# Performance work log

Hardware: AMD Instinct MI355X
Metric: run time of the kernel (lower is better)

The kernel has to match this reference:

```python
import jax, jax.numpy as jnp
import numpy as np

HEADS = 16


def setup_inputs() -> dict:
    key = jax.random.key(0)
    k1, k2, k3 = jax.random.split(key, 3)
    B, T, D = 2, 2048, 1024
    x = jax.random.normal(k1, (B, T, D), dtype=jnp.float32)
    # causal mask, broadcast over batch and heads
    mask = jnp.tril(jnp.ones((T, T), dtype=bool))[None, None, :, :]
    # torch Linear(dim, 3*dim, bias=False): weight [3D, D]; we store transposed [D, 3D]
    Wqkv = jax.random.normal(k2, (D, 3 * D), dtype=jnp.float32) * (D ** -0.5)
    Wo = jax.random.normal(k3, (D, D), dtype=jnp.float32) * (D ** -0.5)
    return {"x": x, "mask": mask, "Wqkv": Wqkv, "Wo": Wo}


def reference(x, mask, Wqkv, Wo):
    B, T, D = x.shape
    h = HEADS
    dh = D // h
    scale = dh ** -0.5
    qkv = (x @ Wqkv).reshape(B, T, 3, h, dh)
    qkv = jnp.transpose(qkv, (2, 0, 3, 1, 4))  # [3, B, h, T, dh]
    q, k, v = qkv[0], qkv[1], qkv[2]
    att = jnp.einsum("bhqd,bhkd->bhqk", q, k) * scale  # [B, h, T, T]
    att = jnp.where(mask, att, jnp.float32(-1e9))
    att = jax.nn.softmax(att, axis=-1)
    # dropout: identity in eval/reference mode
    out = jnp.einsum("bhqk,bhkd->bhqd", att, v)  # [B, h, T, dh]
    out = jnp.transpose(out, (0, 2, 1, 3)).reshape(B, T, D)
    return out @ Wo
```

## Files before the change

kernel.cpp:

```cpp
#include <hip/hip_runtime.h>
#include <cstdint>

typedef unsigned short ushort_t;
typedef __attribute__((ext_vector_type(8))) short short8;
typedef __attribute__((ext_vector_type(4))) float f32x4;

#define B_ 2
#define T_ 2048
#define D_ 1024
#define H_ 16
#define DH_ 64

__device__ inline unsigned short f2bf(float f) {
  unsigned int u = __float_as_uint(f);
  u += 0x7FFF + ((u >> 16) & 1);
  return (unsigned short)(u >> 16);
}

__device__ inline unsigned short f2bf_fast(float f) {
  return (unsigned short)((__float_as_uint(f) + 0x8000u) >> 16);
}

__device__ inline f32x4 mfma16(short8 a, short8 b, f32x4 c) {
  return __builtin_amdgcn_mfma_f32_16x16x32_bf16(a, b, c, 0, 0, 0);
}

__device__ inline void gload16(const void* g, void* l) {
  __builtin_amdgcn_global_load_lds(
      (const __attribute__((address_space(1))) unsigned int*)(uintptr_t)g,
      (__attribute__((address_space(3))) unsigned int*)(uint32_t)(uintptr_t)l,
      16, 0, 0);
}

__global__ void k_cvt(const float* __restrict__ in, ushort_t* __restrict__ out, int n4) {
  int i = blockIdx.x * blockDim.x + threadIdx.x;
  if (i >= n4) return;
  float4 v = ((const float4*)in)[i];
  ushort4 o;
  o.x = f2bf(v.x); o.y = f2bf(v.y); o.z = f2bf(v.z); o.w = f2bf(v.w);
  ((ushort4*)out)[i] = o;
}

__global__ void k_tcvt(const float* __restrict__ in, ushort_t* __restrict__ out,
                       int R, int C) {
  __shared__ float tile[32][33];
  int c0 = blockIdx.x * 32, r0 = blockIdx.y * 32;
  int tx = threadIdx.x, ty = threadIdx.y;
#pragma unroll
  for (int i = 0; i < 32; i += 8)
    tile[ty + i][tx] = in[(size_t)(r0 + ty + i) * C + c0 + tx];
  __syncthreads();
#pragma unroll
  for (int i = 0; i < 32; i += 8)
    out[(size_t)(c0 + ty + i) * R + r0 + tx] = f2bf(tile[tx][ty + i]);
}

__global__ void k_pack_qk(const ushort_t* __restrict__ qkv,
                          ushort_t* __restrict__ pq, ushort_t* __restrict__ pk) {
  const int t16 = blockIdx.x, bh = blockIdx.y;
  const int b = bh >> 4, hh = bh & 15;
  const int tsel = threadIdx.x >> 6;
  const int l = threadIdx.x & 63;
  const int lrow = l & 15, lg = l >> 4;
  ushort_t* dst = (tsel ? pk : pq) + (size_t)(bh * 128 + t16) * 1024 + l * 8;
  const ushort_t* src = qkv + (size_t)(b * T_ + t16 * 16 + lrow) * (3 * D_)
                        + tsel * D_ + hh * DH_ + lg * 8;
  short8 v0 = *(const short8*)(src);
  short8 v1 = *(const short8*)(src + 32);
  if (tsel == 0) {
    const float SC = 0.125f * 1.44269504f;
#pragma unroll
    for (int i = 0; i < 8; ++i) {
      float f0 = __uint_as_float(((unsigned)(unsigned short)v0[i]) << 16) * SC;
      float f1 = __uint_as_float(((unsigned)(unsigned short)v1[i]) << 16) * SC;
      v0[i] = (short)f2bf(f0);
      v1[i] = (short)f2bf(f1);
    }
  }
  *(short8*)(dst)       = v0;
  *(short8*)(dst + 512) = v1;
}

__global__ void k_pack_v(const ushort_t* __restrict__ qkv, ushort_t* __restrict__ pv) {
  __shared__ ushort_t tile[32][68];
  const int t32 = blockIdx.x, bh = blockIdx.y;
  const int b = bh >> 4, hh = bh & 15;
  const int t = threadIdx.x;
  {
    const int row = t >> 3, ch = t & 7;
    *(short8*)&tile[row][ch * 8] =
        *(const short8*)(qkv + (size_t)(b * T_ + t32 * 32 + row) * (3 * D_)
                         + 2 * D_ + hh * DH_ + ch * 8);
  }
  __syncthreads();
  const int nt = t >> 6, l = t & 63;
  const int lrow = l & 15, lg = l >> 4;
  const int d = nt * 16 + lrow;
  short8 o;
#pragma unroll
  for (int i = 0; i < 8; ++i) o[i] = (short)tile[lg * 8 + i][d];
  *(short8*)(pv + ((size_t)(bh * 64 + t32) * 4 + nt) * 512 + l * 8) = o;
}

template <int OUTF>
__global__ __launch_bounds__(256, 2) void k_gemm_bt(
    const ushort_t* __restrict__ A, const ushort_t* __restrict__ Bt,
    void* __restrict__ C, int M, int N, int K) {
  __shared__ __align__(16) ushort_t As[128 * 32];
  __shared__ __align__(16) ushort_t Bs[128 * 32];
  const int tid = threadIdx.x;
  const int w = tid >> 6, l = tid & 63;
  const int bm = blockIdx.y, bn = blockIdx.x;
  const int wm = w >> 1, wn = w & 1;

  const f32x4 fz = {0.f, 0.f, 0.f, 0.f};
  f32x4 acc[4][4];
#pragma unroll
  for (int i = 0; i < 4; ++i)
#pragma unroll
    for (int j = 0; j < 4; ++j) acc[i][j] = fz;

  const int r_a = l >> 2;
  const int cb = (l & 3) * 16;
  const int lrow = l & 15;
  const int lk16 = (l >> 4) * 16;

  for (int k0 = 0; k0 < K; k0 += 32) {
    __syncthreads();
#pragma unroll
    for (int c = 0; c < 2; ++c) {
      int row = (w * 2 + c) * 16 + r_a;
      gload16((const char*)A + ((size_t)(bm * 128 + row) * K + k0) * 2 + cb,
              (char*)As + row * 64 + cb);
      gload16((const char*)Bt + ((size_t)(bn * 128 + row) * K + k0) * 2 + cb,
              (char*)Bs + row * 64 + cb);
    }
    __syncthreads();
    short8 af[4], bv[4];
#pragma unroll
    for (int mt = 0; mt < 4; ++mt)
      af[mt] = *(const short8*)((const char*)As + (wm * 64 + mt * 16 + lrow) * 64 + lk16);
#pragma unroll
    for (int nt = 0; nt < 4; ++nt)
      bv[nt] = *(const short8*)((const char*)Bs + (wn * 64 + nt * 16 + lrow) * 64 + lk16);
#pragma unroll
    for (int mt = 0; mt < 4; ++mt)
#pragma unroll
      for (int nt = 0; nt < 4; ++nt)
        acc[mt][nt] = mfma16(af[mt], bv[nt], acc[mt][nt]);
  }

  const int rg = (l >> 4) * 4;
#pragma unroll
  for (int mt = 0; mt < 4; ++mt)
#pragma unroll
    for (int nt = 0; nt < 4; ++nt) {
      size_t col = (size_t)bn * 128 + wn * 64 + nt * 16 + lrow;
#pragma unroll
      for (int r = 0; r < 4; ++r) {
        size_t rowi = (size_t)bm * 128 + wm * 64 + mt * 16 + rg + r;
        if (OUTF)
          ((float*)C)[rowi * N + col] = acc[mt][nt][r];
        else
          ((ushort_t*)C)[rowi * N + col] = f2bf(acc[mt][nt][r]);
      }
    }
}

__global__ __launch_bounds__(128) void k_attn(
    const ushort_t* __restrict__ pq, const ushort_t* __restrict__ pk,
    const ushort_t* __restrict__ pv, ushort_t* __restrict__ ctx) {
  __shared__ __align__(16) ushort_t plds[2][16][72];
  const int tid = threadIdx.x;
  const int w = tid >> 6, l = tid & 63;
  const int n = blockIdx.x;
  const int q = n >> 3;
  const int bh = (n & 7) * 4 + (q & 3);
  const int j = (63 - (q >> 2)) * 2 + w;
  const int b = bh >> 4, hh = bh & 15;
  const int qr0 = j * 16;
  const int lrow = l & 15, lg = l >> 4;

  const ushort_t* pqb = pq + (size_t)(bh * 128 + j) * 1024 + l * 8;
  short8 aq0 = *(const short8*)(pqb);
  short8 aq1 = *(const short8*)(pqb + 512);

  const f32x4 fz = {0.f, 0.f, 0.f, 0.f};
  f32x4 o[4];
#pragma unroll
  for (int nt = 0; nt < 4; ++nt) o[nt] = fz;
  float lsum[4] = {0.f, 0.f, 0.f, 0.f};

  const int ntiles = (j >> 2) + 1;
  for (int t = 0; t < ntiles; ++t) {
    const int kv0 = t * 64;
    const ushort_t* pkb = pk + (size_t)(bh * 128 + (kv0 >> 4)) * 1024 + l * 8;
    short8 bk0[4], bk1[4];
#pragma unroll
    for (int nh = 0; nh < 4; ++nh) {
      bk0[nh] = *(const short8*)(pkb + nh * 1024);
      bk1[nh] = *(const short8*)(pkb + nh * 1024 + 512);
    }
    f32x4 s[4];
    __builtin_amdgcn_s_setprio(1);
#pragma unroll
    for (int nh = 0; nh < 4; ++nh)
      s[nh] = mfma16(aq1, bk1[nh], mfma16(aq0, bk0[nh], fz));
    __builtin_amdgcn_s_setprio(0);
    if (t == ntiles - 1) {
#pragma unroll
      for (int r = 0; r < 4; ++r) {
        int row = qr0 + lg * 4 + r;
#pragma unroll
        for (int nh = 0; nh < 4; ++nh) {
          int col = kv0 + nh * 16 + lrow;
          if (col > row) s[nh][r] = -1e30f;
        }
      }
    }
    const ushort_t* pvb = pv + (size_t)(bh * 64 + (kv0 >> 5)) * 2048 + l * 8;
    short8 bv0[4], bv1[4];
#pragma unroll
    for (int nt = 0; nt < 4; ++nt) {
      bv0[nt] = *(const short8*)(pvb + nt * 512);
      bv1[nt] = *(const short8*)(pvb + 2048 + nt * 512);
    }
#pragma unroll
    for (int r = 0; r < 4; ++r) {
      float p0 = __builtin_amdgcn_exp2f(s[0][r]);
      float p1 = __builtin_amdgcn_exp2f(s[1][r]);
      float p2 = __builtin_amdgcn_exp2f(s[2][r]);
      float p3 = __builtin_amdgcn_exp2f(s[3][r]);
      lsum[r] += (p0 + p1) + (p2 + p3);
      plds[w][lg * 4 + r][lrow]      = f2bf_fast(p0);
      plds[w][lg * 4 + r][16 + lrow] = f2bf_fast(p1);
      plds[w][lg * 4 + r][32 + lrow] = f2bf_fast(p2);
      plds[w][lg * 4 + r][48 + lrow] = f2bf_fast(p3);
    }
    short8 pa0 = *(const short8*)&plds[w][lrow][lg * 8];
    short8 pa1 = *(const short8*)&plds[w][lrow][32 + lg * 8];
    __builtin_amdgcn_s_setprio(1);
#pragma unroll
    for (int nt = 0; nt < 4; ++nt)
      o[nt] = mfma16(pa1, bv1[nt], mfma16(pa0, bv0[nt], o[nt]));
    __builtin_amdgcn_s_setprio(0);
  }
#pragma unroll
  for (int r = 0; r < 4; ++r)
#pragma unroll
    for (int x = 1; x < 16; x <<= 1)
      lsum[r] += __shfl_xor(lsum[r], x);
#pragma unroll
  for (int nt = 0; nt < 4; ++nt) {
#pragma unroll
    for (int r = 0; r < 4; ++r) {
      int row = qr0 + lg * 4 + r;
      ctx[(size_t)(b * T_ + row) * D_ + hh * DH_ + nt * 16 + lrow] =
          f2bf(o[nt][r] / lsum[r]);
    }
  }
}

extern "C" void kernel_launch(void* const* d_in, const int* in_sizes, int n_in,
                              void* d_out, int out_size, void* d_ws, size_t ws_size,
                              hipStream_t stream) {
  const float* x    = (const float*)d_in[0];
  const float* Wqkv = (const float*)d_in[2];
  const float* Wo   = (const float*)d_in[3];
  float* out = (float*)d_out;

  char* ws = (char*)d_ws;
  ushort_t* xb    = (ushort_t*)(ws);
  ushort_t* wqkvT = (ushort_t*)(ws + (8u  << 20));
  ushort_t* woT   = (ushort_t*)(ws + (14u << 20));
  ushort_t* qkvb  = (ushort_t*)(ws + (16u << 20));
  ushort_t* pq    = (ushort_t*)(ws + (40u << 20));
  ushort_t* pk    = (ushort_t*)(ws + (48u << 20));
  ushort_t* pv    = (ushort_t*)(ws);
  ushort_t* ctxb  = (ushort_t*)(ws + (16u << 20));

  dim3 tb(32, 8);
  k_cvt<<<(B_ * T_ * D_) / 4 / 256, 256, 0, stream>>>(x, xb, (B_ * T_ * D_) / 4);
  k_tcvt<<<dim3(96, 32), tb, 0, stream>>>(Wqkv, wqkvT, 1024, 3072);
  k_tcvt<<<dim3(32, 32), tb, 0, stream>>>(Wo, woT, 1024, 1024);
  k_gemm_bt<0><<<dim3(24, 32), 256, 0, stream>>>(xb, wqkvT, qkvb, 4096, 3072, 1024);
  k_pack_qk<<<dim3(128, 32), 128, 0, stream>>>(qkvb, pq, pk);
  k_pack_v<<<dim3(64, 32), 256, 0, stream>>>(qkvb, pv);
  k_attn<<<2048, 128, 0, stream>>>(pq, pk, pv, ctxb);
  k_gemm_bt<1><<<dim3(8, 32), 256, 0, stream>>>(ctxb, woT, out, 4096, 1024, 1024);
}
```

Before: 204.6 us.

## Process two 16-row query tiles per wave in attention to reuse K/V loads

Each wave now handles 32 query rows (two 16-row tiles) instead of 16. Every loaded K and V fragment then feeds twice as many MFMAs, and the grid is halved to 1024 blocks. This cuts global K/V traffic per query row but raises register pressure and halves the number of waves. Causal imbalance also gets coarser, since each wave loops over tiles up to its higher row group and does extra masked work for the first tile.

```diff
diff --git a/kernel.cpp b/kernel.cpp
--- a/kernel.cpp
+++ b/kernel.cpp
@@ -170,28 +170,32 @@
 __global__ __launch_bounds__(128) void k_attn(
     const ushort_t* __restrict__ pq, const ushort_t* __restrict__ pk,
     const ushort_t* __restrict__ pv, ushort_t* __restrict__ ctx) {
-  __shared__ __align__(16) ushort_t plds[2][16][72];
+  __shared__ __align__(16) ushort_t plds[2][2][16][72];
   const int tid = threadIdx.x;
   const int w = tid >> 6, l = tid & 63;
   const int n = blockIdx.x;
   const int q = n >> 3;
   const int bh = (n & 7) * 4 + (q & 3);
-  const int j = (63 - (q >> 2)) * 2 + w;
+  const int j2 = (31 - (q >> 2)) * 2 + w;
   const int b = bh >> 4, hh = bh & 15;
-  const int qr0 = j * 16;
+  const int jlo = j2 * 2;
+  const int qr0 = jlo * 16;
   const int lrow = l & 15, lg = l >> 4;
 
-  const ushort_t* pqb = pq + (size_t)(bh * 128 + j) * 1024 + l * 8;
-  short8 aq0 = *(const short8*)(pqb);
-  short8 aq1 = *(const short8*)(pqb + 512);
+  const ushort_t* pqb = pq + (size_t)(bh * 128 + jlo) * 1024 + l * 8;
+  short8 aq00 = *(const short8*)(pqb);
+  short8 aq01 = *(const short8*)(pqb + 512);
+  short8 aq10 = *(const short8*)(pqb + 1024);
+  short8 aq11 = *(const short8*)(pqb + 1536);
 
   const f32x4 fz = {0.f, 0.f, 0.f, 0.f};
-  f32x4 o[4];
-#pragma unroll
-  for (int nt = 0; nt < 4; ++nt) o[nt] = fz;
-  float lsum[4] = {0.f, 0.f, 0.f, 0.f};
-
-  const int ntiles = (j >> 2) + 1;
+  f32x4 o0[4], o1[4];
+#pragma unroll
+  for (int nt = 0; nt < 4; ++nt) { o0[nt] = fz; o1[nt] = fz; }
+  float ls0[4] = {0.f, 0.f, 0.f, 0.f};
+  float ls1[4] = {0.f, 0.f, 0.f, 0.f};
+
+  const int ntiles = (j2 >> 1) + 1;
   for (int t = 0; t < ntiles; ++t) {
     const int kv0 = t * 64;
     const ushort_t* pkb = pk + (size_t)(bh * 128 + (kv0 >> 4)) * 1024 + l * 8;
@@ -201,20 +205,23 @@
       bk0[nh] = *(const short8*)(pkb + nh * 1024);
       bk1[nh] = *(const short8*)(pkb + nh * 1024 + 512);
     }
-    f32x4 s[4];
+    f32x4 s0[4], s1[4];
     __builtin_amdgcn_s_setprio(1);
 #pragma unroll
-    for (int nh = 0; nh < 4; ++nh)
-      s[nh] = mfma16(aq1, bk1[nh], mfma16(aq0, bk0[nh], fz));
+    for (int nh = 0; nh < 4; ++nh) {
+      s0[nh] = mfma16(aq01, bk1[nh], mfma16(aq00, bk0[nh], fz));
+      s1[nh] = mfma16(aq11, bk1[nh], mfma16(aq10, bk0[nh], fz));
+    }
     __builtin_amdgcn_s_setprio(0);
     if (t == ntiles - 1) {
 #pragma unroll
       for (int r = 0; r < 4; ++r) {
-        int row = qr0 + lg * 4 + r;
+        int row0 = qr0 + lg * 4 + r;
 #pragma unroll
         for (int nh = 0; nh < 4; ++nh) {
           int col = kv0 + nh * 16 + lrow;
-          if (col > row) s[nh][r] = -1e30f;
+          if (col > row0)      s0[nh][r] = -1e30f;
+          if (col > row0 + 16) s1[nh][r] = -1e30f;
         }
       }
     }
@@ -227,36 +234,55 @@
     }
 #pragma unroll
     for (int r = 0; r < 4; ++r) {
-      float p0 = __builtin_amdgcn_exp2f(s[0][r]);
-      float p1 = __builtin_amdgcn_exp2f(s[1][r]);
-      float p2 = __builtin_amdgcn_exp2f(s[2][r]);
-      float p3 = __builtin_amdgcn_exp2f(s[3][r]);
-      lsum[r] += (p0 + p1) + (p2 + p3);
-      plds[w][lg * 4 + r][lrow]      = f2bf_fast(p0);
-      plds[w][lg * 4 + r][16 + lrow] = f2bf_fast(p1);
-      plds[w][lg * 4 + r][32 + lrow] = f2bf_fast(p2);
-      plds[w][lg * 4 + r][48 + lrow] = f2bf_fast(p3);
-    }
-    short8 pa0 = *(const short8*)&plds[w][lrow][lg * 8];
-    short8 pa1 = *(const short8*)&plds[w][lrow][32 + lg * 8];
+      float a0 = __builtin_amdgcn_exp2f(s0[0][r]);
+      float a1 = __builtin_amdgcn_exp2f(s0[1][r]);
+      float a2 = __builtin_amdgcn_exp2f(s0[2][r]);
+      float a3 = __builtin_amdgcn_exp2f(s0[3][r]);
+      float c0 = __builtin_amdgcn_exp2f(s1[0][r]);
+      float c1 = __builtin_amdgcn_exp2f(s1[1][r]);
+      float c2 = __builtin_amdgcn_exp2f(s1[2][r]);
+      float c3 = __builtin_amdgcn_exp2f(s1[3][r]);
+      ls0[r] += (a0 + a1) + (a2 + a3);
+      ls1[r] += (c0 + c1) + (c2 + c3);
+      plds[w][0][lg * 4 + r][lrow]      = f2bf_fast(a0);
+      plds[w][0][lg * 4 + r][16 + lrow] = f2bf_fast(a1);
+      plds[w][0][lg * 4 + r][32 + lrow] = f2bf_fast(a2);
+      plds[w][0][lg * 4 + r][48 + lrow] = f2bf_fast(a3);
+      plds[w][1][lg * 4 + r][lrow]      = f2bf_fast(c0);
+      plds[w][1][lg * 4 + r][16 + lrow] = f2bf_fast(c1);
+      plds[w][1][lg * 4 + r][32 + lrow] = f2bf_fast(c2);
+      plds[w][1][lg * 4 + r][48 + lrow] = f2bf_fast(c3);
+    }
+    short8 pa00 = *(const short8*)&plds[w][0][lrow][lg * 8];
+    short8 pa01 = *(const short8*)&plds[w][0][lrow][32 + lg * 8];
+    short8 pa10 = *(const short8*)&plds[w][1][lrow][lg * 8];
+    short8 pa11 = *(const short8*)&plds[w][1][lrow][32 + lg * 8];
     __builtin_amdgcn_s_setprio(1);
 #pragma unroll
-    for (int nt = 0; nt < 4; ++nt)
-      o[nt] = mfma16(pa1, bv1[nt], mfma16(pa0, bv0[nt], o[nt]));
+    for (int nt = 0; nt < 4; ++nt) {
+      o0[nt] = mfma16(pa01, bv1[nt], mfma16(pa00, bv0[nt], o0[nt]));
+      o1[nt] = mfma16(pa11, bv1[nt], mfma16(pa10, bv0[nt], o1[nt]));
+    }
     __builtin_amdgcn_s_setprio(0);
   }
 #pragma unroll
-  for (int r = 0; r < 4; ++r)
-#pragma unroll
-    for (int x = 1; x < 16; x <<= 1)
-      lsum[r] += __shfl_xor(lsum[r], x);
+  for (int r = 0; r < 4; ++r) {
+#pragma unroll
+    for (int x = 1; x < 16; x <<= 1) {
+      ls0[r] += __shfl_xor(ls0[r], x);
+      ls1[r] += __shfl_xor(ls1[r], x);
+    }
+  }
 #pragma unroll
   for (int nt = 0; nt < 4; ++nt) {
 #pragma unroll
     for (int r = 0; r < 4; ++r) {
-      int row = qr0 + lg * 4 + r;
-      ctx[(size_t)(b * T_ + row) * D_ + hh * DH_ + nt * 16 + lrow] =
-          f2bf(o[nt][r] / lsum[r]);
+      int row0 = qr0 + lg * 4 + r;
+      size_t base = (size_t)b * T_ + row0;
+      ctx[(base) * D_ + hh * DH_ + nt * 16 + lrow] =
+          f2bf(o0[nt][r] / ls0[r]);
+      ctx[(base + 16) * D_ + hh * DH_ + nt * 16 + lrow] =
+          f2bf(o1[nt][r] / ls1[r]);
     }
   }
 }
@@ -286,6 +312,6 @@
   k_gemm_bt<0><<<dim3(24, 32), 256, 0, stream>>>(xb, wqkvT, qkvb, 4096, 3072, 1024);
   k_pack_qk<<<dim3(128, 32), 128, 0, stream>>>(qkvb, pq, pk);
   k_pack_v<<<dim3(64, 32), 256, 0, stream>>>(qkvb, pv);
-  k_attn<<<2048, 128, 0, stream>>>(pq, pk, pv, ctxb);
+  k_attn<<<1024, 128, 0, stream>>>(pq, pk, pv, ctxb);
   k_gemm_bt<1><<<dim3(8, 32), 256, 0, stream>>>(ctxb, woT, out, 4096, 1024, 1024);
 }
```

Measured after the change: 204.3 us. No clear change (-0.1%).
